# Kernel tuning notes

Hardware: AMD Instinct MI355X
Metric: run time of the kernel (lower is better)

The kernel has to match this reference:

```python
import jax, jax.numpy as jnp
import numpy as np
import math

B, L, Z, D, H, NL, K = 32, 64, 32, 512, 8, 8, 8192
DFF = 4 * D
HD = D // H

def _make_pe():
    pos = np.arange(L, dtype=np.float32)[:, None]
    div = np.exp(-math.log(10000.0) * np.arange(0, D, 2, dtype=np.float32) / D)
    pe = np.zeros((L, D), dtype=np.float32)
    pe[:, 0::2] = np.sin(pos * div)
    pe[:, 1::2] = np.cos(pos * div)
    return jnp.asarray(pe)

PE = _make_pe()  # (L, D) sinusoidal positional embedding, max_len = seq_len

def setup_inputs() -> dict:
    key = jax.random.key(0)
    ks = jax.random.split(key, 12)
    s = 0.02
    def rn(k, shape):
        return jax.random.normal(k, shape, jnp.float32) * s
    p = {}
    p["x"] = jax.random.normal(ks[0], (B, L, Z), jnp.float32)
    p["codebook"] = jax.random.normal(ks[1], (K, Z), jnp.float32)
    p["W_in"] = rn(ks[2], (Z, D)); p["b_in"] = jnp.zeros((D,), jnp.float32)
    p["sa_qkv_w"] = rn(ks[3], (NL, D, 3 * D)); p["sa_qkv_b"] = jnp.zeros((NL, 3 * D), jnp.float32)
    p["sa_out_w"] = rn(ks[4], (NL, D, D)); p["sa_out_b"] = jnp.zeros((NL, D), jnp.float32)
    p["ca_qkv_w"] = rn(ks[5], (NL, D, 3 * D)); p["ca_qkv_b"] = jnp.zeros((NL, 3 * D), jnp.float32)
    p["ca_out_w"] = rn(ks[6], (NL, D, D)); p["ca_out_b"] = jnp.zeros((NL, D), jnp.float32)
    p["ff1_w"] = rn(ks[7], (NL, D, DFF)); p["ff1_b"] = jnp.zeros((NL, DFF), jnp.float32)
    p["ff2_w"] = rn(ks[8], (NL, DFF, D)); p["ff2_b"] = jnp.zeros((NL, D), jnp.float32)
    p["ln1_g"] = jnp.ones((NL, D), jnp.float32); p["ln1_b"] = jnp.zeros((NL, D), jnp.float32)
    p["ln2_g"] = jnp.ones((NL, D), jnp.float32); p["ln2_b"] = jnp.zeros((NL, D), jnp.float32)
    p["ln3_g"] = jnp.ones((NL, D), jnp.float32); p["ln3_b"] = jnp.zeros((NL, D), jnp.float32)
    p["ln_g"] = jnp.ones((D,), jnp.float32); p["ln_b"] = jnp.zeros((D,), jnp.float32)
    p["W_out"] = rn(ks[9], (D, Z)); p["b_out"] = jnp.zeros((Z,), jnp.float32)
    return p

def _ln(x, g, b):
    m = x.mean(-1, keepdims=True)
    v = ((x - m) ** 2).mean(-1, keepdims=True)
    return (x - m) / jnp.sqrt(v + 1e-5) * g + b

def _mha(q_in, kv_in, qkv_w, qkv_b, out_w, out_b, key_mask):
    # q_in: (B, Lq, D), kv_in: (B, Lk, D); key_mask: (Lk,) bool or None
    q = q_in @ qkv_w[:, :D] + qkv_b[:D]
    k = kv_in @ qkv_w[:, D:2 * D] + qkv_b[D:2 * D]
    v = kv_in @ qkv_w[:, 2 * D:] + qkv_b[2 * D:]
    split = lambda t: t.reshape(t.shape[0], t.shape[1], H, HD)
    q, k, v = split(q), split(k), split(v)
    s = jnp.einsum('bqhd,bkhd->bhqk', q, k) / math.sqrt(HD)
    if key_mask is not None:
        s = jnp.where(key_mask[None, None, None, :], s, -1e9)
    a = jax.nn.softmax(s, axis=-1)
    o = jnp.einsum('bhqk,bkhd->bqhd', a, v).reshape(q_in.shape)
    return o @ out_w + out_b

def _forward(x, codebook, W_in, b_in, sa_qkv_w, sa_qkv_b, sa_out_w, sa_out_b,
             ca_qkv_w, ca_qkv_b, ca_out_w, ca_out_b, ff1_w, ff1_b, ff2_w, ff2_b,
             ln1_g, ln1_b, ln2_g, ln2_b, ln3_g, ln3_b, ln_g, ln_b, W_out, b_out):
    Bsz = x.shape[0]
    # prepend zero start token -> x_full (B, L+1, Z); context at step i = x_full[:, :i+1]
    x_full = jnp.concatenate([jnp.zeros((Bsz, 1, Z), x.dtype), x], axis=1)
    ctx_h0 = x_full[:, :L] @ W_in + b_in + PE  # padded context, fixed length L

    def step(i):
        key_mask = jnp.arange(L) <= i  # valid context positions 0..i
        # VQ nearest-neighbor quantize of the memory token x_full[:, i+1]
        mem = jnp.take(x_full, i + 1, axis=1)  # (B, Z)
        d2 = ((mem[:, None, :] - codebook[None, :, :]) ** 2).sum(-1)  # (B, K)
        q = jax.lax.stop_gradient(codebook[jnp.argmin(d2, axis=1)])  # (B, Z), detached
        mem_h = (q @ W_in + b_in)[:, None, :]  # (B, 1, D), no pos emb
        h = ctx_h0
        for l in range(NL):  # post-norm TransformerDecoderLayer, relu FFN
            sa = _mha(h, h, sa_qkv_w[l], sa_qkv_b[l], sa_out_w[l], sa_out_b[l], key_mask)
            h = _ln(h + sa, ln1_g[l], ln1_b[l])
            ca = _mha(h, mem_h, ca_qkv_w[l], ca_qkv_b[l], ca_out_w[l], ca_out_b[l], None)
            h = _ln(h + ca, ln2_g[l], ln2_b[l])
            ff = jax.nn.relu(h @ ff1_w[l] + ff1_b[l]) @ ff2_w[l] + ff2_b[l]
            h = _ln(h + ff, ln3_g[l], ln3_b[l])
        pred = _ln(h, ln_g, ln_b) @ W_out + b_out  # (B, L, Z)
        return jnp.take(pred, i, axis=1)  # last valid position (B, Z)

    preds = jax.lax.map(step, jnp.arange(L))  # (L, B, Z)
    return preds.transpose(1, 0, 2)  # (B, L, Z)

def reference(x, codebook, W_in, b_in, sa_qkv_w, sa_qkv_b, sa_out_w, sa_out_b,
              ca_qkv_w, ca_qkv_b, ca_out_w, ca_out_b, ff1_w, ff1_b, ff2_w, ff2_b,
              ln1_g, ln1_b, ln2_g, ln2_b, ln3_g, ln3_b, ln_g, ln_b, W_out, b_out):
    return _forward(x, codebook, W_in, b_in, sa_qkv_w, sa_qkv_b, sa_out_w, sa_out_b,
                    ca_qkv_w, ca_qkv_b, ca_out_w, ca_out_b, ff1_w, ff1_b, ff2_w, ff2_b,
                    ln1_g, ln1_b, ln2_g, ln2_b, ln3_g, ln3_b, ln_g, ln_b, W_out, b_out)
```

## Files before the change

kernel.cpp:

```cpp
#include <hip/hip_runtime.h>
#include <hip/hip_bf16.h>
#include <math.h>
#include <string.h>

#define DEV __device__ __forceinline__

typedef unsigned short u16;
typedef __attribute__((ext_vector_type(8))) short s8v;
typedef __attribute__((ext_vector_type(4))) float f4v;

constexpr int NLAY = 8;
constexpr int SB   = 64 * 32;
constexpr size_t RAGG = 66560;

DEV float bf2f(u16 u) { unsigned x = ((unsigned)u) << 16; union { unsigned u; float f; } c; c.u = x; return c.f; }
DEV u16 f2bf(float f) { union { float f; unsigned u; } c; c.f = f; unsigned x = c.u; x += 0x7fffu + ((x >> 16) & 1u); return (u16)(x >> 16); }

DEV void load8bf(const u16* p, float* o) {
  uint4 q = *(const uint4*)p;
  o[0] = bf2f((u16)(q.x & 0xffff)); o[1] = bf2f((u16)(q.x >> 16));
  o[2] = bf2f((u16)(q.y & 0xffff)); o[3] = bf2f((u16)(q.y >> 16));
  o[4] = bf2f((u16)(q.z & 0xffff)); o[5] = bf2f((u16)(q.z >> 16));
  o[6] = bf2f((u16)(q.w & 0xffff)); o[7] = bf2f((u16)(q.w >> 16));
}
DEV void store8bf(u16* p, const float* v) {
  uint4 q;
  q.x = (unsigned)f2bf(v[0]) | ((unsigned)f2bf(v[1]) << 16);
  q.y = (unsigned)f2bf(v[2]) | ((unsigned)f2bf(v[3]) << 16);
  q.z = (unsigned)f2bf(v[4]) | ((unsigned)f2bf(v[5]) << 16);
  q.w = (unsigned)f2bf(v[6]) | ((unsigned)f2bf(v[7]) << 16);
  *(uint4*)p = q;
}

DEV size_t seqoff(int s, int b) { return (size_t)16 * s * (s + 1) + (size_t)b * (s + 1); }

DEV void cp16(const void* g, void* l) {
  __builtin_amdgcn_global_load_lds((const __attribute__((address_space(1))) unsigned*)g,
                                   (__attribute__((address_space(3))) unsigned*)l, 16, 0, 0);
}

template<int RELU>
__global__ __launch_bounds__(256) void gemm_bt(const u16* __restrict__ A, const u16* __restrict__ Bt,
                                               const float* __restrict__ bias, u16* __restrict__ C,
                                               int N, int K) {
  __shared__ u16 As[128 * 64];
  __shared__ u16 Bs[128 * 64];
  const int tid = threadIdx.x, w = tid >> 6, lane = tid & 63;
  const int lrow = lane & 15, lquad = lane >> 4;
  const int m0 = blockIdx.y * 128, n0 = blockIdx.x * 128;
  const int wm = (w & 1) * 64, wn = (w >> 1) * 64;
  const int srow = lane >> 3, sch = (lane & 7) * 8;
  f4v acc[4][4] = {};
  for (int kt = 0; kt < K; kt += 64) {
    __syncthreads();
#pragma unroll
    for (int c = 0; c < 4; ++c) {
      int seg = w * 4 + c;
      cp16(A + (size_t)(m0 + seg * 8 + srow) * K + kt + sch, &As[seg * 512]);
      cp16(Bt + (size_t)(n0 + seg * 8 + srow) * K + kt + sch, &Bs[seg * 512]);
    }
    __syncthreads();
#pragma unroll
    for (int kc = 0; kc < 2; ++kc) {
      s8v a[4], b[4];
#pragma unroll
      for (int t = 0; t < 4; ++t) {
        a[t] = *(const s8v*)&As[(wm + t * 16 + lrow) * 64 + kc * 32 + lquad * 8];
        b[t] = *(const s8v*)&Bs[(wn + t * 16 + lrow) * 64 + kc * 32 + lquad * 8];
      }
#pragma unroll
      for (int mt = 0; mt < 4; ++mt)
#pragma unroll
        for (int nt = 0; nt < 4; ++nt)
          acc[mt][nt] = __builtin_amdgcn_mfma_f32_16x16x32_bf16(a[mt], b[nt], acc[mt][nt], 0, 0, 0);
    }
  }
#pragma unroll
  for (int nt = 0; nt < 4; ++nt) {
    int col = n0 + wn + nt * 16 + lrow;
    float bv = bias[col];
#pragma unroll
    for (int mt = 0; mt < 4; ++mt) {
      size_t rbase = (size_t)(m0 + wm + mt * 16 + lquad * 4);
#pragma unroll
      for (int j = 0; j < 4; ++j) {
        float v = acc[mt][nt][j] + bv;
        if (RELU) v = fmaxf(v, 0.f);
        C[(rbase + j) * (size_t)N + col] = f2bf(v);
      }
    }
  }
}

__global__ __launch_bounds__(256) void gemm_ca(const u16* __restrict__ A0, const u16* __restrict__ Bt0,
                                               const float* __restrict__ bias0, u16* __restrict__ C0,
                                               size_t sA, size_t sB, int sBias, size_t sC) {
  const int z = blockIdx.z;
  const u16* A = A0 + sA * z;
  const u16* Bt = Bt0 + sB * z;
  const float* bias = bias0 + (size_t)sBias * z;
  u16* C = C0 + sC * z;
  const int N = 512, K = 512;
  __shared__ u16 As[128 * 64];
  __shared__ u16 Bs[128 * 64];
  const int tid = threadIdx.x, w = tid >> 6, lane = tid & 63;
  const int lrow = lane & 15, lquad = lane >> 4;
  const int m0 = blockIdx.y * 128, n0 = blockIdx.x * 128;
  const int wm = (w & 1) * 64, wn = (w >> 1) * 64;
  const int srow = lane >> 3, sch = (lane & 7) * 8;
  f4v acc[4][4] = {};
  for (int kt = 0; kt < K; kt += 64) {
    __syncthreads();
#pragma unroll
    for (int c = 0; c < 4; ++c) {
      int seg = w * 4 + c;
      cp16(A + (size_t)(m0 + seg * 8 + srow) * K + kt + sch, &As[seg * 512]);
      cp16(Bt + (size_t)(n0 + seg * 8 + srow) * K + kt + sch, &Bs[seg * 512]);
    }
    __syncthreads();
#pragma unroll
    for (int kc = 0; kc < 2; ++kc) {
      s8v a[4], b[4];
#pragma unroll
      for (int t = 0; t < 4; ++t) {
        a[t] = *(const s8v*)&As[(wm + t * 16 + lrow) * 64 + kc * 32 + lquad * 8];
        b[t] = *(const s8v*)&Bs[(wn + t * 16 + lrow) * 64 + kc * 32 + lquad * 8];
      }
#pragma unroll
      for (int mt = 0; mt < 4; ++mt)
#pragma unroll
        for (int nt = 0; nt < 4; ++nt)
          acc[mt][nt] = __builtin_amdgcn_mfma_f32_16x16x32_bf16(a[mt], b[nt], acc[mt][nt], 0, 0, 0);
    }
  }
#pragma unroll
  for (int nt = 0; nt < 4; ++nt) {
    int col = n0 + wn + nt * 16 + lrow;
    float bv = bias[col];
#pragma unroll
    for (int mt = 0; mt < 4; ++mt) {
      size_t rbase = (size_t)(m0 + wm + mt * 16 + lquad * 4);
#pragma unroll
      for (int j = 0; j < 4; ++j)
        C[(rbase + j) * (size_t)N + col] = f2bf(acc[mt][nt][j] + bv);
    }
  }
}

__global__ __launch_bounds__(256) void k_attn(const u16* __restrict__ qkv, u16* __restrict__ o,
                                              int sbase, size_t row0) {
  const int h = blockIdx.x, b = blockIdx.y, sl = blockIdx.z;
  const int s = sbase + sl;
  const size_t soff = seqoff(s, b) - row0;
  __shared__ u16 qs[64][72], ks[64][72], vts[64][72], ps[64][72];
  const int tid = threadIdx.x;
  const int row = tid >> 2, c16 = (tid & 3) * 16;
  const int rcl = row <= s ? row : s;
  {
    const u16* qp = qkv + (soff + rcl) * 1536 + h * 64 + c16;
    *(uint4*)&qs[row][c16]     = *(const uint4*)qp;
    *(uint4*)&qs[row][c16 + 8] = *(const uint4*)(qp + 8);
    *(uint4*)&ks[row][c16]     = *(const uint4*)(qp + 512);
    *(uint4*)&ks[row][c16 + 8] = *(const uint4*)(qp + 520);
    uint4 v0 = *(const uint4*)(qp + 1024), v1 = *(const uint4*)(qp + 1032);
    unsigned arr[8] = {v0.x, v0.y, v0.z, v0.w, v1.x, v1.y, v1.z, v1.w};
#pragma unroll
    for (int j = 0; j < 8; ++j) {
      vts[c16 + 2 * j][row]     = (u16)(arr[j] & 0xffff);
      vts[c16 + 2 * j + 1][row] = (u16)(arr[j] >> 16);
    }
  }
  __syncthreads();
  const int w = tid >> 6, lane = tid & 63, lrow = lane & 15, lquad = lane >> 4;
  f4v sc[4] = {};
  {
    s8v aq[2];
#pragma unroll
    for (int kc = 0; kc < 2; ++kc) aq[kc] = *(const s8v*)&qs[w * 16 + lrow][kc * 32 + lquad * 8];
#pragma unroll
    for (int nt = 0; nt < 4; ++nt)
#pragma unroll
      for (int kc = 0; kc < 2; ++kc) {
        s8v bk = *(const s8v*)&ks[nt * 16 + lrow][kc * 32 + lquad * 8];
        sc[nt] = __builtin_amdgcn_mfma_f32_16x16x32_bf16(aq[kc], bk, sc[nt], 0, 0, 0);
      }
  }
#pragma unroll
  for (int j = 0; j < 4; ++j) {
    float v[4]; float mx = -3.0e38f;
#pragma unroll
    for (int nt = 0; nt < 4; ++nt) {
      int col = nt * 16 + lrow;
      float xx = sc[nt][j] * 0.125f;
      if (col > s) xx = -1e9f;
      v[nt] = xx; mx = fmaxf(mx, xx);
    }
#pragma unroll
    for (int m = 1; m < 16; m <<= 1) mx = fmaxf(mx, __shfl_xor(mx, m));
    float sum = 0.f;
#pragma unroll
    for (int nt = 0; nt < 4; ++nt) { v[nt] = __expf(v[nt] - mx); sum += v[nt]; }
#pragma unroll
    for (int m = 1; m < 16; m <<= 1) sum += __shfl_xor(sum, m);
    float inv = 1.f / sum;
    int prow = w * 16 + lquad * 4 + j;
#pragma unroll
    for (int nt = 0; nt < 4; ++nt) ps[prow][nt * 16 + lrow] = f2bf(v[nt] * inv);
  }
  f4v oc[4] = {};
  {
    s8v ap[2];
#pragma unroll
    for (int kc = 0; kc < 2; ++kc) ap[kc] = *(const s8v*)&ps[w * 16 + lrow][kc * 32 + lquad * 8];
#pragma unroll
    for (int nt = 0; nt < 4; ++nt)
#pragma unroll
      for (int kc = 0; kc < 2; ++kc) {
        s8v bv = *(const s8v*)&vts[nt * 16 + lrow][kc * 32 + lquad * 8];
        oc[nt] = __builtin_amdgcn_mfma_f32_16x16x32_bf16(ap[kc], bv, oc[nt], 0, 0, 0);
      }
  }
#pragma unroll
  for (int nt = 0; nt < 4; ++nt) {
    int col = h * 64 + nt * 16 + lrow;
#pragma unroll
    for (int j = 0; j < 4; ++j) {
      int r = w * 16 + lquad * 4 + j;
      if (r <= s) o[(soff + r) * 512 + col] = f2bf(oc[nt][j]);
    }
  }
}

__global__ __launch_bounds__(64) void k_attn_last(const u16* __restrict__ qb, const u16* __restrict__ kvb,
                                                  u16* __restrict__ attl, int sbase, size_t row0) {
  const int h = blockIdx.x;
  const int r = blockIdx.y;
  const int sl = r >> 5, b = r & 31;
  const int s = sbase + sl;
  const size_t soff = seqoff(s, b) - row0;
  const int lane = threadIdx.x;
  __shared__ float qsm[64], ps[64];
  qsm[lane] = bf2f(qb[(size_t)r * 512 + h * 64 + lane]);
  __syncthreads();
  float sc = -3.0e38f;
  if (lane <= s) {
    const u16* kp = kvb + (soff + lane) * 1024 + h * 64;
    float acc = 0.f;
#pragma unroll
    for (int d = 0; d < 64; d += 8) {
      float kv[8]; load8bf(kp + d, kv);
#pragma unroll
      for (int i = 0; i < 8; ++i) acc += qsm[d + i] * kv[i];
    }
    sc = acc * 0.125f;
  }
  float mx = sc;
#pragma unroll
  for (int m = 1; m < 64; m <<= 1) mx = fmaxf(mx, __shfl_xor(mx, m));
  float e = (lane <= s) ? __expf(sc - mx) : 0.f;
  float sum = e;
#pragma unroll
  for (int m = 1; m < 64; m <<= 1) sum += __shfl_xor(sum, m);
  ps[lane] = e / sum;
  __syncthreads();
  float acc = 0.f;
  for (int k = 0; k <= s; ++k)
    acc += ps[k] * bf2f(kvb[(soff + k) * 1024 + 512 + h * 64 + lane]);
  attl[(size_t)r * 512 + h * 64 + lane] = f2bf(acc);
}

template<int HAS2>
__global__ __launch_bounds__(256) void k_ln(u16* __restrict__ hb, const u16* __restrict__ tmpb,
                                            const u16* __restrict__ cab, const int* __restrict__ map,
                                            size_t row0,
                                            const float* __restrict__ g1, const float* __restrict__ b1,
                                            const float* __restrict__ g2, const float* __restrict__ b2) {
  const int row = blockIdx.x * 4 + (threadIdx.x >> 6);
  const int lane = threadIdx.x & 63;
  const size_t off = (size_t)row * 512 + lane * 8;
  float hv[8], tv[8], t[8];
  load8bf(hb + off, hv); load8bf(tmpb + off, tv);
  float s = 0.f, ss = 0.f;
#pragma unroll
  for (int i = 0; i < 8; ++i) { t[i] = hv[i] + tv[i]; s += t[i]; ss += t[i] * t[i]; }
#pragma unroll
  for (int m = 1; m < 64; m <<= 1) { s += __shfl_xor(s, m); ss += __shfl_xor(ss, m); }
  float mean = s * (1.f / 512.f);
  float inv = 1.f / sqrtf(ss * (1.f / 512.f) - mean * mean + 1e-5f);
  float gv[8], bv[8];
  *(float4*)&gv[0] = *(const float4*)(g1 + lane * 8); *(float4*)&gv[4] = *(const float4*)(g1 + lane * 8 + 4);
  *(float4*)&bv[0] = *(const float4*)(b1 + lane * 8); *(float4*)&bv[4] = *(const float4*)(b1 + lane * 8 + 4);
  if (HAS2) {
    const int seq = map[row0 + row];
    float cv[8]; load8bf(cab + (size_t)seq * 512 + lane * 8, cv);
    float s2 = 0.f, ss2 = 0.f;
#pragma unroll
    for (int i = 0; i < 8; ++i) { float n = (t[i] - mean) * inv * gv[i] + bv[i] + cv[i]; t[i] = n; s2 += n; ss2 += n * n; }
#pragma unroll
    for (int m = 1; m < 64; m <<= 1) { s2 += __shfl_xor(s2, m); ss2 += __shfl_xor(ss2, m); }
    float mean2 = s2 * (1.f / 512.f);
    float inv2 = 1.f / sqrtf(ss2 * (1.f / 512.f) - mean2 * mean2 + 1e-5f);
    float g2v[8], b2v[8];
    *(float4*)&g2v[0] = *(const float4*)(g2 + lane * 8); *(float4*)&g2v[4] = *(const float4*)(g2 + lane * 8 + 4);
    *(float4*)&b2v[0] = *(const float4*)(b2 + lane * 8); *(float4*)&b2v[4] = *(const float4*)(b2 + lane * 8 + 4);
#pragma unroll
    for (int i = 0; i < 8; ++i) t[i] = (t[i] - mean2) * inv2 * g2v[i] + b2v[i];
  } else {
#pragma unroll
    for (int i = 0; i < 8; ++i) t[i] = (t[i] - mean) * inv * gv[i] + bv[i];
  }
  store8bf(hb + off, t);
}

template<int HAS2>
__global__ __launch_bounds__(256) void k_ln_last(u16* __restrict__ gl, const u16* __restrict__ tmpl,
                                                 const u16* __restrict__ cab, int sbase,
                                                 const float* __restrict__ g1, const float* __restrict__ b1,
                                                 const float* __restrict__ g2, const float* __restrict__ b2) {
  const int row = blockIdx.x * 4 + (threadIdx.x >> 6);
  const int lane = threadIdx.x & 63;
  const size_t off = (size_t)row * 512 + lane * 8;
  float hv[8], tv[8], t[8];
  load8bf(gl + off, hv); load8bf(tmpl + off, tv);
  float s = 0.f, ss = 0.f;
#pragma unroll
  for (int i = 0; i < 8; ++i) { t[i] = hv[i] + tv[i]; s += t[i]; ss += t[i] * t[i]; }
#pragma unroll
  for (int m = 1; m < 64; m <<= 1) { s += __shfl_xor(s, m); ss += __shfl_xor(ss, m); }
  float mean = s * (1.f / 512.f);
  float inv = 1.f / sqrtf(ss * (1.f / 512.f) - mean * mean + 1e-5f);
  float gv[8], bv[8];
  *(float4*)&gv[0] = *(const float4*)(g1 + lane * 8); *(float4*)&gv[4] = *(const float4*)(g1 + lane * 8 + 4);
  *(float4*)&bv[0] = *(const float4*)(b1 + lane * 8); *(float4*)&bv[4] = *(const float4*)(b1 + lane * 8 + 4);
  if (HAS2) {
    const int seq = (sbase + (row >> 5)) * 32 + (row & 31);
    float cv[8]; load8bf(cab + (size_t)seq * 512 + lane * 8, cv);
    float s2 = 0.f, ss2 = 0.f;
#pragma unroll
    for (int i = 0; i < 8; ++i) { float n = (t[i] - mean) * inv * gv[i] + bv[i] + cv[i]; t[i] = n; s2 += n; ss2 += n * n; }
#pragma unroll
    for (int m = 1; m < 64; m <<= 1) { s2 += __shfl_xor(s2, m); ss2 += __shfl_xor(ss2, m); }
    float mean2 = s2 * (1.f / 512.f);
    float inv2 = 1.f / sqrtf(ss2 * (1.f / 512.f) - mean2 * mean2 + 1e-5f);
    float g2v[8], b2v[8];
    *(float4*)&g2v[0] = *(const float4*)(g2 + lane * 8); *(float4*)&g2v[4] = *(const float4*)(g2 + lane * 8 + 4);
    *(float4*)&b2v[0] = *(const float4*)(b2 + lane * 8); *(float4*)&b2v[4] = *(const float4*)(b2 + lane * 8 + 4);
#pragma unroll
    for (int i = 0; i < 8; ++i) t[i] = (t[i] - mean2) * inv2 * g2v[i] + b2v[i];
  } else {
#pragma unroll
    for (int i = 0; i < 8; ++i) t[i] = (t[i] - mean) * inv * gv[i] + bv[i];
  }
  store8bf(gl + off, t);
}

__global__ __launch_bounds__(256) void k_ctx(const float* __restrict__ x, const float* __restrict__ W_in,
                                             const float* __restrict__ b_in, u16* __restrict__ ctx0) {
  const int e = blockIdx.x * 256 + threadIdx.x;
  const int d = e & 511, l = (e >> 9) & 63, b = e >> 15;
  float acc = b_in[d];
  if (l > 0) {
    const float* xr = x + (size_t)(b * 64 + l - 1) * 32;
    float a0 = 0.f, a1 = 0.f, a2 = 0.f, a3 = 0.f;
#pragma unroll
    for (int z = 0; z < 32; z += 4) {
      a0 += xr[z + 0] * W_in[(z + 0) * 512 + d];
      a1 += xr[z + 1] * W_in[(z + 1) * 512 + d];
      a2 += xr[z + 2] * W_in[(z + 2) * 512 + d];
      a3 += xr[z + 3] * W_in[(z + 3) * 512 + d];
    }
    acc += (a0 + a1) + (a2 + a3);
  }
  const float dv = __expf(-9.210340371976184f * (float)(d & ~1) * (1.f / 512.f));
  const float ang = (float)l * dv;
  acc += (d & 1) ? cosf(ang) : sinf(ang);
  ctx0[(size_t)e] = f2bf(acc);
}

__global__ __launch_bounds__(64) void k_map(int* __restrict__ map) {
  const int seq = blockIdx.x;
  const int s = seq >> 5, b = seq & 31;
  const int l = threadIdx.x;
  if (l <= s) map[seqoff(s, b) + l] = seq;
}

__global__ __launch_bounds__(256) void k_rep(const u16* __restrict__ ctx0, u16* __restrict__ hb,
                                             int sbase, size_t row0) {
  const int sl = blockIdx.x >> 5, b = blockIdx.x & 31;
  const int s = sbase + sl;
  const size_t dst0 = seqoff(s, b) - row0;
  const int tid = threadIdx.x;
  for (int idx = tid; idx < (s + 1) * 64; idx += 256) {
    const int l = idx >> 6, d8 = idx & 63;
    *(uint4*)(hb + (dst0 + l) * 512 + d8 * 8) =
        *(const uint4*)(ctx0 + ((size_t)(b * 64 + l) * 512) + d8 * 8);
  }
}

__global__ __launch_bounds__(64) void k_gather(const u16* __restrict__ hb, u16* __restrict__ gl,
                                               int sbase, size_t row0) {
  const int r = blockIdx.x; const int sl = r >> 5, b = r & 31; const int s = sbase + sl;
  const size_t src = (seqoff(s, b) - row0 + s) * 512;
  const int lane = threadIdx.x;
  *(uint4*)(gl + (size_t)r * 512 + lane * 8) = *(const uint4*)(hb + src + lane * 8);
}

__global__ __launch_bounds__(256) void k_vq(const float* __restrict__ x, const float* __restrict__ cb,
                                            const float* __restrict__ W_in, const float* __restrict__ b_in,
                                            u16* __restrict__ memh) {
  __shared__ float cs[128 * 36];
  __shared__ float xs[8][33];
  const int tid = threadIdx.x;
  const int g = tid >> 5, u = tid & 31;
  const int tok = blockIdx.x * 8 + g;
  const int s = tok >> 5, b = tok & 31;
  xs[g][u] = x[(size_t)(b * 64 + s) * 32 + u];
  __syncthreads();
  float xr[32];
#pragma unroll
  for (int i = 0; i < 32; ++i) xr[i] = xs[g][i];
  unsigned long long bk = ~0ull;
  for (int tile = 0; tile < 64; ++tile) {
    __syncthreads();
    const float4* src = (const float4*)(cb + (size_t)tile * 128 * 32);
#pragma unroll
    for (int k = 0; k < 4; ++k) {
      int f4 = k * 256 + tid;
      int c = f4 >> 3, z = (f4 & 7) * 4;
      *(float4*)&cs[c * 36 + z] = src[f4];
    }
    __syncthreads();
#pragma unroll
    for (int j = 0; j < 4; ++j) {
      int c = j * 32 + u;
      const float* cp = &cs[c * 36];
      float d0 = 0.f, d1 = 0.f, d2 = 0.f, d3 = 0.f;
#pragma unroll
      for (int z4 = 0; z4 < 8; ++z4) {
        float4 cv = *(const float4*)(cp + z4 * 4);
        float t0 = xr[z4 * 4 + 0] - cv.x, t1 = xr[z4 * 4 + 1] - cv.y;
        float t2 = xr[z4 * 4 + 2] - cv.z, t3 = xr[z4 * 4 + 3] - cv.w;
        d0 += t0 * t0; d1 += t1 * t1; d2 += t2 * t2; d3 += t3 * t3;
      }
      float d = (d0 + d1) + (d2 + d3);
      unsigned db; memcpy(&db, &d, 4);
      unsigned long long key = ((unsigned long long)db << 32) | (unsigned)(tile * 128 + c);
      bk = key < bk ? key : bk;
    }
  }
#pragma unroll
  for (int m = 1; m < 32; m <<= 1) {
    unsigned long long o = __shfl_xor(bk, m);
    bk = o < bk ? o : bk;
  }
  const int kmin = (int)(bk & 0xffffffffu);
  float cw[32];
#pragma unroll
  for (int z = 0; z < 32; ++z) cw[z] = cb[(size_t)kmin * 32 + z];
  for (int k = 0; k < 16; ++k) {
    int o = u + 32 * k;
    float a = b_in[o];
#pragma unroll
    for (int z = 0; z < 32; ++z) a += cw[z] * W_in[z * 512 + o];
    memh[(size_t)tok * 512 + o] = f2bf(a);
  }
}

__global__ __launch_bounds__(64) void k_final(const u16* __restrict__ gl, const float* __restrict__ g,
                                              const float* __restrict__ bta, const float* __restrict__ Wout,
                                              const float* __restrict__ bout, float* __restrict__ out,
                                              int sbase) {
  const int blk = blockIdx.x;
  const int s = sbase + (blk >> 5), b = blk & 31;
  const int lane = threadIdx.x;
  __shared__ float ns[512];
  const size_t roff = (size_t)blk * 512;
  float v[8]; load8bf(gl + roff + lane * 8, v);
  float sm = 0.f, ssm = 0.f;
#pragma unroll
  for (int i = 0; i < 8; ++i) { sm += v[i]; ssm += v[i] * v[i]; }
#pragma unroll
  for (int m = 1; m < 64; m <<= 1) { sm += __shfl_xor(sm, m); ssm += __shfl_xor(ssm, m); }
  float mean = sm * (1.f / 512.f);
  float inv = 1.f / sqrtf(ssm * (1.f / 512.f) - mean * mean + 1e-5f);
#pragma unroll
  for (int i = 0; i < 8; ++i) ns[lane * 8 + i] = (v[i] - mean) * inv * g[lane * 8 + i] + bta[lane * 8 + i];
  __syncthreads();
  const int col = lane & 31, half = lane >> 5;
  float a = 0.f;
  for (int k = half * 256; k < half * 256 + 256; ++k) a += ns[k] * Wout[(size_t)k * 32 + col];
  a += __shfl_xor(a, 32);
  if (lane < 32) out[((size_t)b * 64 + s) * 32 + col] = a + bout[col];
}

__global__ void k_tcast(const float* __restrict__ src, u16* __restrict__ dst, int R, int C, int ld, int col0) {
  const int l = blockIdx.z;
  src += (size_t)l * R * ld;
  dst += (size_t)l * R * C;
  __shared__ float t[32][33];
  const int c0 = blockIdx.x * 32, r0 = blockIdx.y * 32;
  const int tx = threadIdx.x, ty = threadIdx.y;
#pragma unroll
  for (int k = 0; k < 4; ++k)
    t[ty + 8 * k][tx] = src[(size_t)(r0 + ty + 8 * k) * ld + col0 + c0 + tx];
  __syncthreads();
#pragma unroll
  for (int k = 0; k < 4; ++k)
    dst[(size_t)(c0 + ty + 8 * k) * R + r0 + tx] = f2bf(t[tx][ty + 8 * k]);
}

extern "C" void kernel_launch(void* const* d_in, const int* in_sizes, int n_in,
                              void* d_out, int out_size, void* d_ws, size_t ws_size,
                              hipStream_t stream) {
  (void)in_sizes; (void)n_in; (void)out_size;
  const float* x    = (const float*)d_in[0];
  const float* cb   = (const float*)d_in[1];
  const float* W_in = (const float*)d_in[2];
  const float* b_in = (const float*)d_in[3];
  const float* saqw = (const float*)d_in[4];
  const float* saqb = (const float*)d_in[5];
  const float* saow = (const float*)d_in[6];
  const float* saob = (const float*)d_in[7];
  const float* caqw = (const float*)d_in[8];
  const float* caqb = (const float*)d_in[9];
  const float* caow = (const float*)d_in[10];
  const float* caob = (const float*)d_in[11];
  const float* f1w  = (const float*)d_in[12];
  const float* f1b  = (const float*)d_in[13];
  const float* f2w  = (const float*)d_in[14];
  const float* f2b  = (const float*)d_in[15];
  const float* l1g  = (const float*)d_in[16];
  const float* l1b  = (const float*)d_in[17];
  const float* l2g  = (const float*)d_in[18];
  const float* l2b  = (const float*)d_in[19];
  const float* l3g  = (const float*)d_in[20];
  const float* l3b  = (const float*)d_in[21];
  const float* lng  = (const float*)d_in[22];
  const float* lnb  = (const float*)d_in[23];
  const float* Wout = (const float*)d_in[24];
  const float* bout = (const float*)d_in[25];
  float* out = (float*)d_out;

  u16* ws = (u16*)d_ws;
  size_t off = 0;
  auto alloc = [&](size_t n) { u16* p = ws + off; off += n; return p; };
  u16* ctx0  = alloc((size_t)32 * 64 * 512);
  u16* cabuf = alloc((size_t)NLAY * SB * 512);
  u16* memh  = alloc((size_t)SB * 512);
  u16* tmpv8 = alloc((size_t)NLAY * SB * 512);
  u16* wqkvT = alloc((size_t)NLAY * 1536 * 512);
  u16* woutT = alloc((size_t)NLAY * 512 * 512);
  u16* wf1T  = alloc((size_t)NLAY * 2048 * 512);
  u16* wf2T  = alloc((size_t)NLAY * 512 * 2048);
  u16* wcavT = alloc((size_t)NLAY * 512 * 512);
  u16* wcaoT = alloc((size_t)NLAY * 512 * 512);
  int* rowmap = (int*)alloc(RAGG * 2);

  u16* glast = tmpv8;
  u16* qb    = tmpv8 + 1048576;
  u16* attl  = tmpv8 + 2 * 1048576;
  u16* tmpl  = tmpv8 + 3 * 1048576;
  u16* midl  = tmpv8 + 4 * 1048576;

  size_t avail = ws_size / 2 > off ? ws_size / 2 - off : 0;
  size_t Ralloc = avail / 3072;
  Ralloc = Ralloc / 128 * 128;
  if (Ralloc > RAGG) Ralloc = RAGG;

  u16* hb   = alloc(Ralloc * 512);
  u16* regA = alloc(Ralloc * 2048);
  u16* tmpb = alloc(Ralloc * 512);
  u16* qkvb = regA;
  u16* attb = regA + Ralloc * 1536;
  u16* midb = regA;
  u16* kvb  = regA;

  dim3 tb(32, 8);
  k_tcast<<<dim3(48, 16, 8), tb, 0, stream>>>(saqw, wqkvT, 512, 1536, 1536, 0);
  k_tcast<<<dim3(16, 16, 8), tb, 0, stream>>>(saow, woutT, 512, 512, 512, 0);
  k_tcast<<<dim3(64, 16, 8), tb, 0, stream>>>(f1w, wf1T, 512, 2048, 2048, 0);
  k_tcast<<<dim3(16, 64, 8), tb, 0, stream>>>(f2w, wf2T, 2048, 512, 512, 0);
  k_tcast<<<dim3(16, 16, 8), tb, 0, stream>>>(caqw, wcavT, 512, 512, 1536, 1024);
  k_tcast<<<dim3(16, 16, 8), tb, 0, stream>>>(caow, wcaoT, 512, 512, 512, 0);

  k_ctx<<<4096, 256, 0, stream>>>(x, W_in, b_in, ctx0);
  k_vq<<<256, 256, 0, stream>>>(x, cb, W_in, b_in, memh);
  k_map<<<2048, 64, 0, stream>>>(rowmap);

  gemm_ca<<<dim3(4, 16, 8), 256, 0, stream>>>(memh, wcavT, caqb + 1024, tmpv8,
                                              0, (size_t)512 * 512, 1536, (size_t)SB * 512);
  gemm_ca<<<dim3(4, 16, 8), 256, 0, stream>>>(tmpv8, wcaoT, caob, cabuf,
                                              (size_t)SB * 512, (size_t)512 * 512, 512, (size_t)SB * 512);

  int sstart = 0;
  while (sstart < 64) {
    int send = sstart;
    size_t rows = 0;
    while (send < 64) {
      size_t nr = rows + (size_t)32 * (send + 1);
      size_t pr = (nr + 127) / 128 * 128;
      if (pr > Ralloc && send > sstart) break;
      rows = nr; ++send;
      if (pr > Ralloc) break;
    }
    const size_t row0 = (size_t)16 * sstart * (sstart + 1);
    const size_t rows_pad = (rows + 127) / 128 * 128;
    const int mg = (int)(rows_pad / 128);
    const int ns = send - sstart;
    const int nseq = ns * 32;
    const int nseqp = (nseq + 127) / 128 * 128;

    k_rep<<<nseq, 256, 0, stream>>>(ctx0, hb, sstart, row0);
    for (int l = 0; l < NLAY - 1; ++l) {
      gemm_bt<0><<<dim3(12, mg), 256, 0, stream>>>(hb, wqkvT + (size_t)l * 1536 * 512,
                                                   saqb + (size_t)l * 1536, qkvb, 1536, 512);
      k_attn<<<dim3(8, 32, ns), 256, 0, stream>>>(qkvb, attb, sstart, row0);
      gemm_bt<0><<<dim3(4, mg), 256, 0, stream>>>(attb, woutT + (size_t)l * 512 * 512,
                                                  saob + (size_t)l * 512, tmpb, 512, 512);
      k_ln<1><<<(int)(rows / 4), 256, 0, stream>>>(hb, tmpb, cabuf + (size_t)l * SB * 512,
                                                   rowmap, row0,
                                                   l1g + l * 512, l1b + l * 512, l2g + l * 512, l2b + l * 512);
      gemm_bt<1><<<dim3(16, mg), 256, 0, stream>>>(hb, wf1T + (size_t)l * 2048 * 512,
                                                   f1b + (size_t)l * 2048, midb, 2048, 512);
      gemm_bt<0><<<dim3(4, mg), 256, 0, stream>>>(midb, wf2T + (size_t)l * 512 * 2048,
                                                  f2b + (size_t)l * 512, tmpb, 512, 2048);
      k_ln<0><<<(int)(rows / 4), 256, 0, stream>>>(hb, tmpb, nullptr, rowmap, row0,
                                                   l3g + l * 512, l3b + l * 512, nullptr, nullptr);
    }
    {
      const size_t l7q = (size_t)7 * 1536 * 512;
      k_gather<<<nseq, 64, 0, stream>>>(hb, glast, sstart, row0);
      gemm_bt<0><<<dim3(8, mg), 256, 0, stream>>>(hb, wqkvT + l7q + (size_t)512 * 512,
                                                  saqb + 7 * 1536 + 512, kvb, 1024, 512);
      gemm_bt<0><<<dim3(4, nseqp / 128), 256, 0, stream>>>(glast, wqkvT + l7q,
                                                           saqb + 7 * 1536, qb, 512, 512);
      k_attn_last<<<dim3(8, nseq), 64, 0, stream>>>(qb, kvb, attl, sstart, row0);
      gemm_bt<0><<<dim3(4, nseqp / 128), 256, 0, stream>>>(attl, woutT + (size_t)7 * 512 * 512,
                                                           saob + 7 * 512, tmpl, 512, 512);
      k_ln_last<1><<<nseq / 4, 256, 0, stream>>>(glast, tmpl, cabuf + (size_t)7 * SB * 512, sstart,
                                                 l1g + 7 * 512, l1b + 7 * 512, l2g + 7 * 512, l2b + 7 * 512);
      gemm_bt<1><<<dim3(16, nseqp / 128), 256, 0, stream>>>(glast, wf1T + (size_t)7 * 2048 * 512,
                                                            f1b + (size_t)7 * 2048, midl, 2048, 512);
      gemm_bt<0><<<dim3(4, nseqp / 128), 256, 0, stream>>>(midl, wf2T + (size_t)7 * 512 * 2048,
                                                           f2b + 7 * 512, tmpl, 512, 2048);
      k_ln_last<0><<<nseq / 4, 256, 0, stream>>>(glast, tmpl, nullptr, sstart,
                                                 l3g + 7 * 512, l3b + 7 * 512, nullptr, nullptr);
      k_final<<<nseq, 64, 0, stream>>>(glast, lng, lnb, Wout, bout, out, sstart);
    }
    sstart = send;
  }
}
```

Before: 7.414 ms.

## Fuse residual add into GEMM epilogue and split VQ argmin across codebook chunks

The residual add now happens in the GEMM epilogue through a RES template flag, so the layernorm kernels read only the summed buffer and skip one input load per row. Separately, the VQ nearest-codebook search is split across 8 codebook chunks per token block. Each chunk merges its best match with a 64-bit atomicMin on a packed distance and index key, and a second kernel projects the chosen code through W_in. This adds parallelism to what was a 256-block kernel, at the cost of a memset, atomics and an extra launch. The epilogue now does scattered, non-vectorised residual reads.

```diff
diff --git a/kernel.cpp b/kernel.cpp
--- a/kernel.cpp
+++ b/kernel.cpp
@@ -6,6 +6,7 @@
 #define DEV __device__ __forceinline__
 
 typedef unsigned short u16;
+typedef unsigned long long u64;
 typedef __attribute__((ext_vector_type(8))) short s8v;
 typedef __attribute__((ext_vector_type(4))) float f4v;
 
@@ -39,10 +40,10 @@
                                    (__attribute__((address_space(3))) unsigned*)l, 16, 0, 0);
 }
 
-template<int RELU>
+template<int RELU, int RES>
 __global__ __launch_bounds__(256) void gemm_bt(const u16* __restrict__ A, const u16* __restrict__ Bt,
                                                const float* __restrict__ bias, u16* __restrict__ C,
-                                               int N, int K) {
+                                               const u16* __restrict__ res, int N, int K) {
   __shared__ u16 As[128 * 64];
   __shared__ u16 Bs[128 * 64];
   const int tid = threadIdx.x, w = tid >> 6, lane = tid & 63;
@@ -86,6 +87,7 @@
       for (int j = 0; j < 4; ++j) {
         float v = acc[mt][nt][j] + bv;
         if (RELU) v = fmaxf(v, 0.f);
+        if (RES) v += bf2f(res[(rbase + j) * (size_t)N + col]);
         C[(rbase + j) * (size_t)N + col] = f2bf(v);
       }
     }
@@ -278,11 +280,11 @@
   const int row = blockIdx.x * 4 + (threadIdx.x >> 6);
   const int lane = threadIdx.x & 63;
   const size_t off = (size_t)row * 512 + lane * 8;
-  float hv[8], tv[8], t[8];
-  load8bf(hb + off, hv); load8bf(tmpb + off, tv);
+  float t[8];
+  load8bf(tmpb + off, t);
   float s = 0.f, ss = 0.f;
 #pragma unroll
-  for (int i = 0; i < 8; ++i) { t[i] = hv[i] + tv[i]; s += t[i]; ss += t[i] * t[i]; }
+  for (int i = 0; i < 8; ++i) { s += t[i]; ss += t[i] * t[i]; }
 #pragma unroll
   for (int m = 1; m < 64; m <<= 1) { s += __shfl_xor(s, m); ss += __shfl_xor(ss, m); }
   float mean = s * (1.f / 512.f);
@@ -320,11 +322,11 @@
   const int row = blockIdx.x * 4 + (threadIdx.x >> 6);
   const int lane = threadIdx.x & 63;
   const size_t off = (size_t)row * 512 + lane * 8;
-  float hv[8], tv[8], t[8];
-  load8bf(gl + off, hv); load8bf(tmpl + off, tv);
+  float t[8];
+  load8bf(tmpl + off, t);
   float s = 0.f, ss = 0.f;
 #pragma unroll
-  for (int i = 0; i < 8; ++i) { t[i] = hv[i] + tv[i]; s += t[i]; ss += t[i] * t[i]; }
+  for (int i = 0; i < 8; ++i) { s += t[i]; ss += t[i] * t[i]; }
 #pragma unroll
   for (int m = 1; m < 64; m <<= 1) { s += __shfl_xor(s, m); ss += __shfl_xor(ss, m); }
   float mean = s * (1.f / 512.f);
@@ -405,24 +407,25 @@
   *(uint4*)(gl + (size_t)r * 512 + lane * 8) = *(const uint4*)(hb + src + lane * 8);
 }
 
-__global__ __launch_bounds__(256) void k_vq(const float* __restrict__ x, const float* __restrict__ cb,
-                                            const float* __restrict__ W_in, const float* __restrict__ b_in,
-                                            u16* __restrict__ memh) {
+__global__ __launch_bounds__(256) void k_vq_min(const float* __restrict__ x, const float* __restrict__ cb,
+                                                u64* __restrict__ keys) {
   __shared__ float cs[128 * 36];
   __shared__ float xs[8][33];
   const int tid = threadIdx.x;
   const int g = tid >> 5, u = tid & 31;
   const int tok = blockIdx.x * 8 + g;
   const int s = tok >> 5, b = tok & 31;
+  const int chunk = blockIdx.y;
   xs[g][u] = x[(size_t)(b * 64 + s) * 32 + u];
   __syncthreads();
   float xr[32];
 #pragma unroll
   for (int i = 0; i < 32; ++i) xr[i] = xs[g][i];
-  unsigned long long bk = ~0ull;
-  for (int tile = 0; tile < 64; ++tile) {
+  u64 bk = ~0ull;
+  for (int tile = 0; tile < 8; ++tile) {
     __syncthreads();
-    const float4* src = (const float4*)(cb + (size_t)tile * 128 * 32);
+    const int cbase = chunk * 1024 + tile * 128;
+    const float4* src = (const float4*)(cb + (size_t)cbase * 32);
 #pragma unroll
     for (int k = 0; k < 4; ++k) {
       int f4 = k * 256 + tid;
@@ -444,25 +447,37 @@
       }
       float d = (d0 + d1) + (d2 + d3);
       unsigned db; memcpy(&db, &d, 4);
-      unsigned long long key = ((unsigned long long)db << 32) | (unsigned)(tile * 128 + c);
+      u64 key = ((u64)db << 32) | (unsigned)(cbase + c);
       bk = key < bk ? key : bk;
     }
   }
 #pragma unroll
   for (int m = 1; m < 32; m <<= 1) {
-    unsigned long long o = __shfl_xor(bk, m);
+    u64 o = __shfl_xor(bk, m);
     bk = o < bk ? o : bk;
   }
-  const int kmin = (int)(bk & 0xffffffffu);
-  float cw[32];
-#pragma unroll
-  for (int z = 0; z < 32; ++z) cw[z] = cb[(size_t)kmin * 32 + z];
-  for (int k = 0; k < 16; ++k) {
-    int o = u + 32 * k;
-    float a = b_in[o];
-#pragma unroll
-    for (int z = 0; z < 32; ++z) a += cw[z] * W_in[z * 512 + o];
-    memh[(size_t)tok * 512 + o] = f2bf(a);
+  if (u == 0) atomicMin(&keys[tok], bk);
+}
+
+__global__ __launch_bounds__(256) void k_vq_emit(const u64* __restrict__ keys, const float* __restrict__ cb,
+                                                 const float* __restrict__ W_in, const float* __restrict__ b_in,
+                                                 u16* __restrict__ memh) {
+  const int tok = blockIdx.x;
+  const int tid = threadIdx.x;
+  __shared__ float cs[32];
+  const int kmin = (int)(keys[tok] & 0xffffffffu);
+  if (tid < 32) cs[tid] = cb[(size_t)kmin * 32 + tid];
+  __syncthreads();
+  for (int o = tid; o < 512; o += 256) {
+    float a0 = b_in[o], a1 = 0.f, a2 = 0.f, a3 = 0.f;
+#pragma unroll
+    for (int z = 0; z < 32; z += 4) {
+      a0 += cs[z + 0] * W_in[(z + 0) * 512 + o];
+      a1 += cs[z + 1] * W_in[(z + 1) * 512 + o];
+      a2 += cs[z + 2] * W_in[(z + 2) * 512 + o];
+      a3 += cs[z + 3] * W_in[(z + 3) * 512 + o];
+    }
+    memh[(size_t)tok * 512 + o] = f2bf((a0 + a1) + (a2 + a3));
   }
 }
 
@@ -555,6 +570,7 @@
   u16* wcavT = alloc((size_t)NLAY * 512 * 512);
   u16* wcaoT = alloc((size_t)NLAY * 512 * 512);
   int* rowmap = (int*)alloc(RAGG * 2);
+  u64* keys  = (u64*)alloc((size_t)SB * 4);
 
   u16* glast = tmpv8;
   u16* qb    = tmpv8 + 1048576;
@@ -584,7 +600,9 @@
   k_tcast<<<dim3(16, 16, 8), tb, 0, stream>>>(caow, wcaoT, 512, 512, 512, 0);
 
   k_ctx<<<4096, 256, 0, stream>>>(x, W_in, b_in, ctx0);
-  k_vq<<<256, 256, 0, stream>>>(x, cb, W_in, b_in, memh);
+  hipMemsetAsync(keys, 0xFF, (size_t)SB * 8, stream);
+  k_vq_min<<<dim3(256, 8), 256, 0, stream>>>(x, cb, keys);
+  k_vq_emit<<<SB, 256, 0, stream>>>(keys, cb, W_in, b_in, memh);
   k_map<<<2048, 64, 0, stream>>>(rowmap);
 
   gemm_ca<<<dim3(4, 16, 8), 256, 0, stream>>>(memh, wcavT, caqb + 1024, tmpv8,
@@ -612,37 +630,37 @@
 
     k_rep<<<nseq, 256, 0, stream>>>(ctx0, hb, sstart, row0);
     for (int l = 0; l < NLAY - 1; ++l) {
-      gemm_bt<0><<<dim3(12, mg), 256, 0, stream>>>(hb, wqkvT + (size_t)l * 1536 * 512,
-                                                   saqb + (size_t)l * 1536, qkvb, 1536, 512);
+      gemm_bt<0, 0><<<dim3(12, mg), 256, 0, stream>>>(hb, wqkvT + (size_t)l * 1536 * 512,
+                                                      saqb + (size_t)l * 1536, qkvb, nullptr, 1536, 512);
       k_attn<<<dim3(8, 32, ns), 256, 0, stream>>>(qkvb, attb, sstart, row0);
-      gemm_bt<0><<<dim3(4, mg), 256, 0, stream>>>(attb, woutT + (size_t)l * 512 * 512,
-                                                  saob + (size_t)l * 512, tmpb, 512, 512);
+      gemm_bt<0, 1><<<dim3(4, mg), 256, 0, stream>>>(attb, woutT + (size_t)l * 512 * 512,
+                                                     saob + (size_t)l * 512, tmpb, hb, 512, 512);
       k_ln<1><<<(int)(rows / 4), 256, 0, stream>>>(hb, tmpb, cabuf + (size_t)l * SB * 512,
                                                    rowmap, row0,
                                                    l1g + l * 512, l1b + l * 512, l2g + l * 512, l2b + l * 512);
-      gemm_bt<1><<<dim3(16, mg), 256, 0, stream>>>(hb, wf1T + (size_t)l * 2048 * 512,
-                                                   f1b + (size_t)l * 2048, midb, 2048, 512);
-      gemm_bt<0><<<dim3(4, mg), 256, 0, stream>>>(midb, wf2T + (size_t)l * 512 * 2048,
-                                                  f2b + (size_t)l * 512, tmpb, 512, 2048);
+      gemm_bt<1, 0><<<dim3(16, mg), 256, 0, stream>>>(hb, wf1T + (size_t)l * 2048 * 512,
+                                                      f1b + (size_t)l * 2048, midb, nullptr, 2048, 512);
+      gemm_bt<0, 1><<<dim3(4, mg), 256, 0, stream>>>(midb, wf2T + (size_t)l * 512 * 2048,
+                                                     f2b + (size_t)l * 512, tmpb, hb, 512, 2048);
       k_ln<0><<<(int)(rows / 4), 256, 0, stream>>>(hb, tmpb, nullptr, rowmap, row0,
                                                    l3g + l * 512, l3b + l * 512, nullptr, nullptr);
     }
     {
       const size_t l7q = (size_t)7 * 1536 * 512;
       k_gather<<<nseq, 64, 0, stream>>>(hb, glast, sstart, row0);
-      gemm_bt<0><<<dim3(8, mg), 256, 0, stream>>>(hb, wqkvT + l7q + (size_t)512 * 512,
-                                                  saqb + 7 * 1536 + 512, kvb, 1024, 512);
-      gemm_bt<0><<<dim3(4, nseqp / 128), 256, 0, stream>>>(glast, wqkvT + l7q,
-                                                           saqb + 7 * 1536, qb, 512, 512);
+      gemm_bt<0, 0><<<dim3(8, mg), 256, 0, stream>>>(hb, wqkvT + l7q + (size_t)512 * 512,
+                                                     saqb + 7 * 1536 + 512, kvb, nullptr, 1024, 512);
+      gemm_bt<0, 0><<<dim3(4, nseqp / 128), 256, 0, stream>>>(glast, wqkvT + l7q,
+                                                              saqb + 7 * 1536, qb, nullptr, 512, 512);
       k_attn_last<<<dim3(8, nseq), 64, 0, stream>>>(qb, kvb, attl, sstart, row0);
-      gemm_bt<0><<<dim3(4, nseqp / 128), 256, 0, stream>>>(attl, woutT + (size_t)7 * 512 * 512,
-                                                           saob + 7 * 512, tmpl, 512, 512);
+      gemm_bt<0, 1><<<dim3(4, nseqp / 128), 256, 0, stream>>>(attl, woutT + (size_t)7 * 512 * 512,
+                                                              saob + 7 * 512, tmpl, glast, 512, 512);
       k_ln_last<1><<<nseq / 4, 256, 0, stream>>>(glast, tmpl, cabuf + (size_t)7 * SB * 512, sstart,
                                                  l1g + 7 * 512, l1b + 7 * 512, l2g + 7 * 512, l2b + 7 * 512);
-      gemm_bt<1><<<dim3(16, nseqp / 128), 256, 0, stream>>>(glast, wf1T + (size_t)7 * 2048 * 512,
-                                                            f1b + (size_t)7 * 2048, midl, 2048, 512);
-      gemm_bt<0><<<dim3(4, nseqp / 128), 256, 0, stream>>>(midl, wf2T + (size_t)7 * 512 * 2048,
-                                                           f2b + 7 * 512, tmpl, 512, 2048);
+      gemm_bt<1, 0><<<dim3(16, nseqp / 128), 256, 0, stream>>>(glast, wf1T + (size_t)7 * 2048 * 512,
+                                                               f1b + (size_t)7 * 2048, midl, nullptr, 2048, 512);
+      gemm_bt<0, 1><<<dim3(4, nseqp / 128), 256, 0, stream>>>(midl, wf2T + (size_t)7 * 512 * 2048,
+                                                              f2b + 7 * 512, tmpl, glast, 512, 2048);
       k_ln_last<0><<<nseq / 4, 256, 0, stream>>>(glast, tmpl, nullptr, sstart,
                                                  l3g + 7 * 512, l3b + 7 * 512, nullptr, nullptr);
       k_final<<<nseq, 64, 0, stream>>>(glast, lng, lnb, Wout, bout, out, sstart);
```

New measurement: 7.539 ms. Within noise of the previous version (+1.7%).
